# Performance work log

Hardware: AMD Instinct MI355X
Metric: run time of the kernel (lower is better)

The kernel has to match this reference:

```python
import jax, jax.numpy as jnp
import numpy as np

B, L, D, N = 2, 2048, 1024, 16
H = D // N  # head dim 64
MASK_FILL = -100000000.0  # torch code uses -1e8 for non-fp16


def sinusoidal_pos(seq_len, dim):
    # interleaved (sin, cos) table, shape (seq_len, dim); identical per head
    inv_freq = 1.0 / (10000.0 ** (jnp.arange(0, dim, 2, dtype=jnp.float32) / dim))
    ang = jnp.arange(seq_len, dtype=jnp.float32)[:, None] * inv_freq[None, :]
    return jnp.stack([jnp.sin(ang), jnp.cos(ang)], axis=-1).reshape(seq_len, dim)


def apply_rope(x, pos_emb):
    # x: (b, n, l, h); pos_emb: (l, h) interleaved sin/cos
    cos = jnp.repeat(pos_emb[..., 1::2], 2, axis=-1)  # (l, h)
    sin = jnp.repeat(pos_emb[..., ::2], 2, axis=-1)
    x2 = jnp.stack([-x[..., 1::2], x[..., ::2]], axis=-1).reshape(x.shape)
    return x * cos + x2 * sin


def setup_inputs() -> dict:
    key = jax.random.key(0)
    ks = jax.random.split(key, 12)
    inp = {
        "q": jax.random.normal(ks[0], (B, L, D), dtype=jnp.float32),
        "k": jax.random.normal(ks[1], (B, L, D), dtype=jnp.float32),
        "v": jax.random.normal(ks[2], (B, L, D), dtype=jnp.float32),
        "mask": jax.random.bernoulli(ks[3], 0.3, (B, L)),  # True = masked
    }
    s = 0.02
    for i, name in enumerate(["q", "k", "v", "o"]):
        inp[f"W{name}"] = jax.random.normal(ks[4 + i], (D, D), dtype=jnp.float32) * s
        inp[f"b{name}"] = jax.random.normal(ks[8 + i], (D,), dtype=jnp.float32) * s
    return inp


def reference(q, k, v, mask, Wq, bq, Wk, bk, Wv, bv, Wo, bo):
    # projections (torch Linear: x @ W^T + b) and head split -> (b, n, l, h)
    def split_heads(x):
        return x.reshape(B, L, N, H).transpose(0, 2, 1, 3)

    qw = split_heads(q @ Wq.T + bq)
    kw = split_heads(k @ Wk.T + bk)
    vw = split_heads(v @ Wv.T + bv)

    pos = sinusoidal_pos(L, H)
    qw = apply_rope(qw, pos)
    kw = apply_rope(kw, pos)

    # NOTE: original scales by sqrt(hidden_dim), not sqrt(head_dim)
    scores = jnp.einsum("bnlh,bnph->bnlp", qw, kw) / np.sqrt(D).astype(np.float32)
    scores = jnp.where(mask[:, None, None, :], MASK_FILL, scores)
    attn = jax.nn.softmax(scores, axis=-1)  # dropout is identity in eval

    out = jnp.einsum("bnlp,bnph->bnlh", attn, vw)  # (b, n, l, h)
    out = out.transpose(0, 2, 1, 3).reshape(B, L, D)
    return out @ Wo.T + bo
```

## Files before the change

kernel.cpp:

```cpp
#include <hip/hip_runtime.h>
#include <stdint.h>

#define L_SEQ 2048
#define DMODEL 1024
#define NHEAD 16
#define HDIM 64
#define BATCH 2

typedef __attribute__((ext_vector_type(8))) short bf16x8;
typedef __attribute__((ext_vector_type(4))) float f32x4;

#define MFMA(a, b, c) __builtin_amdgcn_mfma_f32_16x16x32_bf16((a), (b), (c), 0, 0, 0)

#if __has_builtin(__builtin_amdgcn_exp2f)
#define EXP2(x) __builtin_amdgcn_exp2f(x)
#else
#define EXP2(x) exp2f(x)
#endif

#if __has_builtin(__builtin_amdgcn_wave_barrier)
#define WAVE_FENCE() __builtin_amdgcn_wave_barrier()
#else
#define WAVE_FENCE() __syncthreads()
#endif

#define QSCALE 0.04508422f
#define MASKBIAS -100.0f

__device__ __forceinline__ unsigned short f2bf(float f) {
    return (unsigned short)((__float_as_uint(f) + 0x8000u) >> 16);
}
__device__ __forceinline__ float bf2f(unsigned short h) {
    return __uint_as_float(((unsigned int)h) << 16);
}
__device__ __forceinline__ unsigned int pkbf(float a, float b) {
    return __builtin_amdgcn_perm(__float_as_uint(b) + 0x8000u,
                                 __float_as_uint(a) + 0x8000u, 0x07060302u);
}
__device__ __forceinline__ void gl2lds16(const unsigned short* g, unsigned short* l) {
    __builtin_amdgcn_global_load_lds(
        (const __attribute__((address_space(1))) void*)g,
        (__attribute__((address_space(3))) void*)l, 16, 0, 0);
}

__global__ void prep_kernel(
    const float* __restrict__ q, const float* __restrict__ k, const float* __restrict__ v,
    const float* __restrict__ wq, const float* __restrict__ wk, const float* __restrict__ wv,
    const float* __restrict__ Wo, const int* __restrict__ mask,
    unsigned short* __restrict__ xb, unsigned short* __restrict__ wb,
    unsigned short* __restrict__ whi, unsigned short* __restrict__ wlo,
    float2* __restrict__ ropetab, float* __restrict__ fbias)
{
    const int y = blockIdx.y, x = blockIdx.x, tid = threadIdx.x;
    if (y < 6) {
        const float* src = (y == 0) ? q : (y == 1) ? k : (y == 2) ? v
                         : (y == 3) ? wq : (y == 4) ? wk : wv;
        unsigned short* dst = (y < 3) ? xb + (size_t)y * 4194304
                                      : wb + (size_t)(y - 3) * 1048576;
        const int n = (y < 3) ? 4194304 : 1048576;
        const int i = (x * 256 + tid) * 8;
        if (i >= n) return;
        const float4 a = *(const float4*)(src + i);
        const float4 b = *(const float4*)(src + i + 4);
        uint4 u;
        u.x = pkbf(a.x, a.y); u.y = pkbf(a.z, a.w);
        u.z = pkbf(b.x, b.y); u.w = pkbf(b.z, b.w);
        *(uint4*)(dst + i) = u;
    } else if (y == 6) {
        const int i = (x * 256 + tid) * 4;
        if (i >= DMODEL * DMODEL) return;
        const float4 vv = *(const float4*)(Wo + i);
        const float f[4] = {vv.x, vv.y, vv.z, vv.w};
        union { unsigned short s[4]; uint2 u; } h, l;
#pragma unroll
        for (int r = 0; r < 4; ++r) {
            h.s[r] = f2bf(f[r]);
            l.s[r] = f2bf(f[r] - bf2f(h.s[r]));
        }
        *(uint2*)&whi[i] = h.u;
        *(uint2*)&wlo[i] = l.u;
    } else {
        if (x < 512) {
            const int idx = x * 256 + tid;
            const int l = idx >> 6, h = idx & 63;
            const float invf = powf(10000.0f, -(float)(h & 62) * (1.0f / 64.0f));
            float sn, cs;
            sincosf((float)l * invf, &sn, &cs);
            ropetab[idx] = make_float2(cs, sn);
        } else if (x < 528) {
            const int idx = (x - 512) * 256 + tid;
            fbias[idx] = (mask[idx] != 0) ? MASKBIAS : 0.0f;
        }
    }
}

__global__ __launch_bounds__(256) void qkv_kernel(
    const unsigned short* __restrict__ Xb, const unsigned short* __restrict__ Wb,
    const float* __restrict__ bq, const float* __restrict__ bk, const float* __restrict__ bv,
    const float2* __restrict__ ropetab,
    unsigned short* __restrict__ Qd, unsigned short* __restrict__ Kd,
    unsigned short* __restrict__ Vd)
{
    const int id = blockIdx.x;
    const int bx = id / 96, rem = id % 96;
    const int z = rem >> 5, by = rem & 31;

    const unsigned short* X = Xb + (size_t)z * (BATCH * L_SEQ * DMODEL);
    const unsigned short* W = Wb + (size_t)z * (DMODEL * DMODEL);
    const float* bias = (z == 0) ? bq : (z == 1) ? bk : bv;

    __shared__ __align__(16) unsigned short As[128 * 64];
    __shared__ __align__(16) unsigned short Bs[128 * 64];

    const int tid  = threadIdx.x;
    const int wave = tid >> 6, lane = tid & 63;
    const int ml = lane & 15, kq = lane >> 4;
    const int m0 = by * 128, n0 = bx * 128;
    const int wm = (wave & 1) * 64, wn = (wave >> 1) * 64;

    f32x4 acc[4][4];
#pragma unroll
    for (int i = 0; i < 4; ++i)
#pragma unroll
        for (int j = 0; j < 4; ++j) acc[i][j] = (f32x4){0.f, 0.f, 0.f, 0.f};

    const int prow = wave * 32 + (lane >> 3);
    const int pch  = (lane & 7) ^ ((lane >> 3) & 7);
    const unsigned short* gA = X + (size_t)(m0 + prow) * DMODEL + pch * 8;
    const unsigned short* gB = W + (size_t)(n0 + prow) * DMODEL + pch * 8;
    unsigned short* lA = As + wave * 2048;
    unsigned short* lB = Bs + wave * 2048;

    for (int kc = 0; kc < DMODEL; kc += 64) {
#pragma unroll
        for (int qq = 0; qq < 4; ++qq) {
            gl2lds16(gA + kc + (size_t)qq * 8 * DMODEL, lA + qq * 512);
            gl2lds16(gB + kc + (size_t)qq * 8 * DMODEL, lB + qq * 512);
        }
        __syncthreads();

        bf16x8 af[2][4], bfv[2][4];
#pragma unroll
        for (int ks = 0; ks < 2; ++ks)
#pragma unroll
            for (int i = 0; i < 4; ++i) {
                const int Ra = wm + i * 16 + ml;
                af[ks][i] = *(const bf16x8*)&As[Ra * 64 + (((ks * 4 + kq) ^ (Ra & 7)) << 3)];
                const int Rb = wn + i * 16 + ml;
                bfv[ks][i] = *(const bf16x8*)&Bs[Rb * 64 + (((ks * 4 + kq) ^ (Rb & 7)) << 3)];
            }
#pragma unroll
        for (int ks = 0; ks < 2; ++ks)
#pragma unroll
            for (int i = 0; i < 4; ++i)
#pragma unroll
                for (int j = 0; j < 4; ++j)
                    acc[i][j] = MFMA(af[ks][i], bfv[ks][j], acc[i][j]);
        __syncthreads();
    }

    if (z < 2) {
        unsigned short* dst = (z == 0) ? Qd : Kd;
        const float osc = (z == 0) ? QSCALE : 1.0f;
#pragma unroll
        for (int jt = 0; jt < 4; ++jt) {
            const int col = n0 + wn + jt * 16 + ml;
            const float bv = bias[col];
            const int nh = col >> 6, hh = col & 63;
            const int odd = hh & 1;
#pragma unroll
            for (int it = 0; it < 4; ++it) {
#pragma unroll
                for (int r = 0; r < 4; ++r) {
                    const int row = m0 + wm + it * 16 + kq * 4 + r;
                    const int bb = row >> 11, ll = row & 2047;
                    const float v = acc[it][jt][r] + bv;
                    const float partner = __shfl_xor(v, 1);
                    const float2 cs = ropetab[ll * 64 + hh];
                    const float res = odd ? fmaf(v, cs.x, partner * cs.y)
                                          : fmaf(v, cs.x, -partner * cs.y);
                    dst[(((size_t)(bb * NHEAD + nh) * L_SEQ + ll) << 6) + hh] = f2bf(res * osc);
                }
            }
        }
    } else {
#pragma unroll
        for (int jt = 0; jt < 4; ++jt) {
            const int col = n0 + wn + jt * 16 + ml;
            const float bv = bias[col];
            const int nh = col >> 6, hh = col & 63;
#pragma unroll
            for (int it = 0; it < 4; ++it) {
                const int rb = m0 + wm + it * 16 + kq * 4;
                const int bb = rb >> 11, ll = rb & 2047;
                uint2 pk;
                pk.x = pkbf(acc[it][jt][0] + bv, acc[it][jt][1] + bv);
                pk.y = pkbf(acc[it][jt][2] + bv, acc[it][jt][3] + bv);
                *(uint2*)&Vd[(((size_t)bb * NHEAD + nh) * HDIM + hh) * L_SEQ + ll] = pk;
            }
        }
    }
}

__global__ __launch_bounds__(256) void attn_kernel(
    const unsigned short* __restrict__ Qr, const unsigned short* __restrict__ Kr,
    const unsigned short* __restrict__ Vt, const float* __restrict__ fbias,
    unsigned short* __restrict__ AOhi, unsigned short* __restrict__ AOlo)
{
    __shared__ __align__(16) unsigned short Ks[2][64 * 64];
    __shared__ __align__(16) unsigned short Vs[2][64 * 64];
    __shared__ __align__(16) unsigned short Ps[4][32 * 64];

    const int tid  = threadIdx.x;
    const int wave = tid >> 6, lane = tid & 63;
    const int ml = lane & 15, kq = lane >> 4;

    const int id = blockIdx.x;
    const int xcd = id & 7, slot = id >> 3;
    const int bh = xcd * 4 + (slot & 3);
    const int qb = slot >> 2;
    const int b = bh >> 4, nh = bh & 15;
    const int q0 = qb * 128;
    const int wq = wave * 32;

    const unsigned short* Qp = Qr + (size_t)bh * L_SEQ * HDIM;
    const unsigned short* Kp = Kr + (size_t)bh * L_SEQ * HDIM;
    const unsigned short* Vp = Vt + (size_t)bh * HDIM * L_SEQ;

    bf16x8 qf[2][2];
#pragma unroll
    for (int qt = 0; qt < 2; ++qt)
#pragma unroll
        for (int c = 0; c < 2; ++c)
            qf[qt][c] = *(const bf16x8*)(Qp + (size_t)(q0 + wq + qt * 16 + ml) * HDIM + c * 32 + kq * 8);

    float li[2] = {0.f, 0.f};
    f32x4 o[2][4];
#pragma unroll
    for (int qt = 0; qt < 2; ++qt)
#pragma unroll
        for (int ht = 0; ht < 4; ++ht) o[qt][ht] = (f32x4){0.f, 0.f, 0.f, 0.f};

    unsigned short* Pw = Ps[wave];

    const int srow8 = lane >> 3;
    const int sch   = (lane & 7) ^ srow8;
    const unsigned short* gK = Kp + (size_t)(wave * 16 + srow8) * HDIM + sch * 8;
    const unsigned short* gV = Vp + (size_t)(wave * 16 + srow8) * L_SEQ + sch * 8;

#define STAGE(kt, bf)                                                          \
    do {                                                                       \
        gl2lds16(gK + (size_t)((kt) * 64) * HDIM, &Ks[bf][(wave * 16) * 64]);  \
        gl2lds16(gK + (size_t)((kt) * 64 + 8) * HDIM,                          \
                 &Ks[bf][(wave * 16 + 8) * 64]);                               \
        gl2lds16(gV + (kt) * 64, &Vs[bf][(wave * 16) * 64]);                   \
        gl2lds16(gV + (size_t)8 * L_SEQ + (kt) * 64,                           \
                 &Vs[bf][(wave * 16 + 8) * 64]);                               \
    } while (0)

    const float* fbp = fbias + (size_t)b * L_SEQ + kq * 4;
    f32x4 bcur[4], bnext[4];
#pragma unroll
    for (int nt = 0; nt < 4; ++nt) bcur[nt] = *(const f32x4*)(fbp + nt * 16);

    STAGE(0, 0);

    for (int kt = 0; kt < L_SEQ / 64; ++kt) {
        const int buf = kt & 1;
        __syncthreads();
        if (kt + 1 < L_SEQ / 64) {
            STAGE(kt + 1, buf ^ 1);
#pragma unroll
            for (int nt = 0; nt < 4; ++nt)
                bnext[nt] = *(const f32x4*)(fbp + (kt + 1) * 64 + nt * 16);
        }

        const unsigned short* Kb = Ks[buf];
        const unsigned short* Vb = Vs[buf];

        f32x4 st[2][4];
#pragma unroll
        for (int nt = 0; nt < 4; ++nt) {
            const int R = nt * 16 + ml;
            const bf16x8 kf0 = *(const bf16x8*)&Kb[R * 64 + ((kq ^ (R & 7)) << 3)];
            const bf16x8 kf1 = *(const bf16x8*)&Kb[R * 64 + (((4 + kq) ^ (R & 7)) << 3)];
#pragma unroll
            for (int qt = 0; qt < 2; ++qt) {
                f32x4 c = MFMA(kf0, qf[qt][0], bcur[nt]);
                c = MFMA(kf1, qf[qt][1], c);
                st[qt][nt] = c;
            }
        }

#pragma unroll
        for (int qt = 0; qt < 2; ++qt) {
#pragma unroll
            for (int nt = 0; nt < 4; ++nt) {
                float p[4];
#pragma unroll
                for (int r = 0; r < 4; ++r) {
                    p[r] = EXP2(st[qt][nt][r]);
                    li[qt] += p[r];
                }
                uint2 pk;
                pk.x = pkbf(p[0], p[1]);
                pk.y = pkbf(p[2], p[3]);
                const int row = qt * 16 + ml;
                const int ck = nt * 2 + (kq >> 1);
                *(uint2*)&Pw[row * 64 + ((ck ^ (ml & 7)) << 3) + (kq & 1) * 4] = pk;
            }
        }
        WAVE_FENCE();

        bf16x8 pf[2][2];
#pragma unroll
        for (int qt = 0; qt < 2; ++qt) {
            const int row = qt * 16 + ml;
            pf[qt][0] = *(const bf16x8*)&Pw[row * 64 + ((kq ^ (ml & 7)) << 3)];
            pf[qt][1] = *(const bf16x8*)&Pw[row * 64 + (((4 + kq) ^ (ml & 7)) << 3)];
        }
#pragma unroll
        for (int ht = 0; ht < 4; ++ht) {
            const int R = ht * 16 + ml;
            const bf16x8 vf0 = *(const bf16x8*)&Vb[R * 64 + ((kq ^ (R & 7)) << 3)];
            const bf16x8 vf1 = *(const bf16x8*)&Vb[R * 64 + (((4 + kq) ^ (R & 7)) << 3)];
#pragma unroll
            for (int qt = 0; qt < 2; ++qt) {
                o[qt][ht] = MFMA(vf0, pf[qt][0], o[qt][ht]);
                o[qt][ht] = MFMA(vf1, pf[qt][1], o[qt][ht]);
            }
        }
        WAVE_FENCE();

#pragma unroll
        for (int nt = 0; nt < 4; ++nt) bcur[nt] = bnext[nt];
    }
#undef STAGE

#pragma unroll
    for (int qt = 0; qt < 2; ++qt) {
        li[qt] += __shfl_xor(li[qt], 16);
        li[qt] += __shfl_xor(li[qt], 32);
    }
    const float inv[2] = {1.f / li[0], 1.f / li[1]};

    const int qr = lane >> 2, quarter = lane & 3;
    const int rc0 = (quarter * 2) ^ (qr & 7), rc1 = (quarter * 2 + 1) ^ (qr & 7);

#pragma unroll
    for (int qt = 0; qt < 2; ++qt)
#pragma unroll
        for (int ht = 0; ht < 4; ++ht) {
            uint2 pk;
            pk.x = pkbf(o[qt][ht][0] * inv[qt], o[qt][ht][1] * inv[qt]);
            pk.y = pkbf(o[qt][ht][2] * inv[qt], o[qt][ht][3] * inv[qt]);
            const int row = qt * 16 + ml;
            const int ck = ht * 2 + (kq >> 1);
            *(uint2*)&Pw[row * 64 + ((ck ^ (ml & 7)) << 3) + (kq & 1) * 4] = pk;
        }
    WAVE_FENCE();
#pragma unroll
    for (int qt = 0; qt < 2; ++qt) {
        const size_t gbase = ((size_t)b * L_SEQ + q0 + wq + qt * 16 + qr) * DMODEL
                             + nh * 64 + quarter * 16;
        const uint4 d0 = *(const uint4*)&Pw[(qt * 16 + qr) * 64 + (rc0 << 3)];
        const uint4 d1 = *(const uint4*)&Pw[(qt * 16 + qr) * 64 + (rc1 << 3)];
        *(uint4*)&AOhi[gbase]     = d0;
        *(uint4*)&AOhi[gbase + 8] = d1;
    }
    WAVE_FENCE();
#pragma unroll
    for (int qt = 0; qt < 2; ++qt)
#pragma unroll
        for (int ht = 0; ht < 4; ++ht) {
            float lo[4];
#pragma unroll
            for (int r = 0; r < 4; ++r) {
                const float v = o[qt][ht][r] * inv[qt];
                const float hf = __uint_as_float((__float_as_uint(v) + 0x8000u) & 0xffff0000u);
                lo[r] = v - hf;
            }
            uint2 pk;
            pk.x = pkbf(lo[0], lo[1]);
            pk.y = pkbf(lo[2], lo[3]);
            const int row = qt * 16 + ml;
            const int ck = ht * 2 + (kq >> 1);
            *(uint2*)&Pw[row * 64 + ((ck ^ (ml & 7)) << 3) + (kq & 1) * 4] = pk;
        }
    WAVE_FENCE();
#pragma unroll
    for (int qt = 0; qt < 2; ++qt) {
        const size_t gbase = ((size_t)b * L_SEQ + q0 + wq + qt * 16 + qr) * DMODEL
                             + nh * 64 + quarter * 16;
        const uint4 d0 = *(const uint4*)&Pw[(qt * 16 + qr) * 64 + (rc0 << 3)];
        const uint4 d1 = *(const uint4*)&Pw[(qt * 16 + qr) * 64 + (rc1 << 3)];
        *(uint4*)&AOlo[gbase]     = d0;
        *(uint4*)&AOlo[gbase + 8] = d1;
    }
}

__global__ __launch_bounds__(256) void oproj_kernel(
    const unsigned short* __restrict__ Ahi_g, const unsigned short* __restrict__ Alo_g,
    const unsigned short* __restrict__ Whi_g, const unsigned short* __restrict__ Wlo_g,
    const float* __restrict__ bias, float* __restrict__ out)
{
    const int id = blockIdx.x;
    const int bxn = id >> 5, by = id & 31;

    __shared__ __align__(16) unsigned short Ah[128 * 32], Al[128 * 32];
    __shared__ __align__(16) unsigned short Bh[64 * 32],  Bl[64 * 32];

    const int tid  = threadIdx.x;
    const int wave = tid >> 6, lane = tid & 63;
    const int ml = lane & 15, kq = lane >> 4;
    const int m0 = by * 128, n0 = bxn * 64;
    const int wm = (wave & 1) * 64, wn = (wave >> 1) * 32;

    f32x4 acc[4][2];
#pragma unroll
    for (int i = 0; i < 4; ++i)
#pragma unroll
        for (int j = 0; j < 2; ++j) acc[i][j] = (f32x4){0.f, 0.f, 0.f, 0.f};

    const int rl  = lane >> 2;
    const int pch = (lane & 3) ^ ((lane >> 3) & 3);
    const int prowA = wave * 32 + rl;
    const int prowB = wave * 16 + rl;
    const unsigned short* gAh = Ahi_g + (size_t)(m0 + prowA) * DMODEL + pch * 8;
    const unsigned short* gAl = Alo_g + (size_t)(m0 + prowA) * DMODEL + pch * 8;
    const unsigned short* gBh = Whi_g + (size_t)(n0 + prowB) * DMODEL + pch * 8;
    const unsigned short* gBl = Wlo_g + (size_t)(n0 + prowB) * DMODEL + pch * 8;
    unsigned short* lAh = Ah + wave * 1024;
    unsigned short* lAl = Al + wave * 1024;
    unsigned short* lBh = Bh + wave * 512;
    unsigned short* lBl = Bl + wave * 512;

    for (int kc = 0; kc < DMODEL; kc += 32) {
#pragma unroll
        for (int qq = 0; qq < 2; ++qq) {
            const size_t go = kc + (size_t)qq * 16 * DMODEL;
            gl2lds16(gAh + go, lAh + qq * 512);
            gl2lds16(gAl + go, lAl + qq * 512);
        }
        gl2lds16(gBh + kc, lBh);
        gl2lds16(gBl + kc, lBl);
        __syncthreads();

        bf16x8 ah[4], al[4], bh_[2], bl_[2];
#pragma unroll
        for (int i = 0; i < 4; ++i) {
            const int Ra = wm + i * 16 + ml;
            const int sa = Ra * 32 + ((kq ^ ((Ra >> 1) & 3)) << 3);
            ah[i] = *(const bf16x8*)&Ah[sa];
            al[i] = *(const bf16x8*)&Al[sa];
        }
#pragma unroll
        for (int j = 0; j < 2; ++j) {
            const int Rb = wn + j * 16 + ml;
            const int sb = Rb * 32 + ((kq ^ ((Rb >> 1) & 3)) << 3);
            bh_[j] = *(const bf16x8*)&Bh[sb];
            bl_[j] = *(const bf16x8*)&Bl[sb];
        }
#pragma unroll
        for (int i = 0; i < 4; ++i)
#pragma unroll
            for (int j = 0; j < 2; ++j) {
                acc[i][j] = MFMA(ah[i], bh_[j], acc[i][j]);
                acc[i][j] = MFMA(al[i], bh_[j], acc[i][j]);
                acc[i][j] = MFMA(ah[i], bl_[j], acc[i][j]);
            }
        __syncthreads();
    }

#pragma unroll
    for (int jt = 0; jt < 2; ++jt) {
        const int col = n0 + wn + jt * 16 + ml;
        const float bv = bias[col];
#pragma unroll
        for (int it = 0; it < 4; ++it)
#pragma unroll
            for (int r = 0; r < 4; ++r) {
                const int row = m0 + wm + it * 16 + kq * 4 + r;
                out[(size_t)row * DMODEL + col] = acc[it][jt][r] + bv;
            }
    }
}

extern "C" void kernel_launch(void* const* d_in, const int* in_sizes, int n_in,
                              void* d_out, int out_size, void* d_ws, size_t ws_size,
                              hipStream_t stream)
{
    (void)in_sizes; (void)n_in; (void)out_size; (void)ws_size;
    const float* q    = (const float*)d_in[0];
    const float* k    = (const float*)d_in[1];
    const float* v    = (const float*)d_in[2];
    const int*   mask = (const int*)d_in[3];
    const float* Wq   = (const float*)d_in[4];
    const float* bq   = (const float*)d_in[5];
    const float* Wk   = (const float*)d_in[6];
    const float* bk   = (const float*)d_in[7];
    const float* Wv   = (const float*)d_in[8];
    const float* bv   = (const float*)d_in[9];
    const float* Wo   = (const float*)d_in[10];
    const float* bo   = (const float*)d_in[11];
    float* out = (float*)d_out;

    const size_t HE = (size_t)BATCH * NHEAD * L_SEQ * HDIM;
    const size_t DD = (size_t)DMODEL * DMODEL;
    unsigned short* Xb   = (unsigned short*)d_ws;
    unsigned short* Wb   = Xb + 3 * HE;
    unsigned short* Qr   = Wb + 3 * DD;
    unsigned short* Kr   = Qr + HE;
    unsigned short* Vt   = Kr + HE;
    unsigned short* Whi  = Vt + HE;
    unsigned short* Wlo  = Whi + DD;
    float* fbias = (float*)(Wlo + DD);
    float2* ropetab = (float2*)(fbias + (size_t)BATCH * L_SEQ);
    unsigned short* AOhi = Xb;
    unsigned short* AOlo = Xb + HE;

    prep_kernel<<<dim3(2048, 8), dim3(256), 0, stream>>>(
        q, k, v, Wq, Wk, Wv, Wo, mask, Xb, Wb, Whi, Wlo, ropetab, fbias);

    qkv_kernel<<<dim3(768), dim3(256), 0, stream>>>(Xb, Wb, bq, bk, bv, ropetab, Qr, Kr, Vt);

    attn_kernel<<<dim3(512), dim3(256), 0, stream>>>(Qr, Kr, Vt, fbias, AOhi, AOlo);

    oproj_kernel<<<dim3(512), dim3(256), 0, stream>>>(AOhi, AOlo, Whi, Wlo, bo, out);
}
```

Before: 248.9 us.

## Split attention over key dimension with atomic accumulation and separate normalize kernel

Result: slower. 351.0 us (+41.1%).

```diff
diff --git a/kernel.cpp b/kernel.cpp
--- a/kernel.cpp
+++ b/kernel.cpp
@@ -6,6 +6,8 @@
 #define NHEAD 16
 #define HDIM 64
 #define BATCH 2
+#define KSPLIT 2
+#define NKT (L_SEQ / 64 / KSPLIT)
 
 typedef __attribute__((ext_vector_type(8))) short bf16x8;
 typedef __attribute__((ext_vector_type(4))) float f32x4;
@@ -94,6 +96,20 @@
     }
 }
 
+__global__ __launch_bounds__(256) void zero_kernel(
+    float* __restrict__ accum, float* __restrict__ liacc)
+{
+    const size_t NA = (size_t)BATCH * NHEAD * L_SEQ * HDIM;
+    const size_t NL = (size_t)BATCH * NHEAD * L_SEQ;
+    const size_t i = ((size_t)blockIdx.x * 256 + threadIdx.x) * 4;
+    if (i < NA) {
+        *(float4*)(accum + i) = make_float4(0.f, 0.f, 0.f, 0.f);
+    } else {
+        const size_t j = i - NA;
+        if (j < NL) *(float4*)(liacc + j) = make_float4(0.f, 0.f, 0.f, 0.f);
+    }
+}
+
 __global__ __launch_bounds__(256) void qkv_kernel(
     const unsigned short* __restrict__ Xb, const unsigned short* __restrict__ Wb,
     const float* __restrict__ bq, const float* __restrict__ bk, const float* __restrict__ bv,
@@ -205,7 +221,7 @@
 __global__ __launch_bounds__(256) void attn_kernel(
     const unsigned short* __restrict__ Qr, const unsigned short* __restrict__ Kr,
     const unsigned short* __restrict__ Vt, const float* __restrict__ fbias,
-    unsigned short* __restrict__ AOhi, unsigned short* __restrict__ AOlo)
+    float* __restrict__ accum, float* __restrict__ liacc)
 {
     __shared__ __align__(16) unsigned short Ks[2][64 * 64];
     __shared__ __align__(16) unsigned short Vs[2][64 * 64];
@@ -216,12 +232,15 @@
     const int ml = lane & 15, kq = lane >> 4;
 
     const int id = blockIdx.x;
-    const int xcd = id & 7, slot = id >> 3;
+    const int sp  = id >> 9;
+    const int rid = id & 511;
+    const int xcd = rid & 7, slot = rid >> 3;
     const int bh = xcd * 4 + (slot & 3);
     const int qb = slot >> 2;
-    const int b = bh >> 4, nh = bh & 15;
+    const int b = bh >> 4;
     const int q0 = qb * 128;
     const int wq = wave * 32;
+    const int koff = sp * (L_SEQ / KSPLIT);
 
     const unsigned short* Qp = Qr + (size_t)bh * L_SEQ * HDIM;
     const unsigned short* Kp = Kr + (size_t)bh * L_SEQ * HDIM;
@@ -245,8 +264,8 @@
 
     const int srow8 = lane >> 3;
     const int sch   = (lane & 7) ^ srow8;
-    const unsigned short* gK = Kp + (size_t)(wave * 16 + srow8) * HDIM + sch * 8;
-    const unsigned short* gV = Vp + (size_t)(wave * 16 + srow8) * L_SEQ + sch * 8;
+    const unsigned short* gK = Kp + (size_t)(koff + wave * 16 + srow8) * HDIM + sch * 8;
+    const unsigned short* gV = Vp + (size_t)(wave * 16 + srow8) * L_SEQ + koff + sch * 8;
 
 #define STAGE(kt, bf)                                                          \
     do {                                                                       \
@@ -258,17 +277,17 @@
                  &Vs[bf][(wave * 16 + 8) * 64]);                               \
     } while (0)
 
-    const float* fbp = fbias + (size_t)b * L_SEQ + kq * 4;
+    const float* fbp = fbias + (size_t)b * L_SEQ + koff + kq * 4;
     f32x4 bcur[4], bnext[4];
 #pragma unroll
     for (int nt = 0; nt < 4; ++nt) bcur[nt] = *(const f32x4*)(fbp + nt * 16);
 
     STAGE(0, 0);
 
-    for (int kt = 0; kt < L_SEQ / 64; ++kt) {
+    for (int kt = 0; kt < NKT; ++kt) {
         const int buf = kt & 1;
         __syncthreads();
-        if (kt + 1 < L_SEQ / 64) {
+        if (kt + 1 < NKT) {
             STAGE(kt + 1, buf ^ 1);
 #pragma unroll
             for (int nt = 0; nt < 4; ++nt)
@@ -342,60 +361,46 @@
         li[qt] += __shfl_xor(li[qt], 16);
         li[qt] += __shfl_xor(li[qt], 32);
     }
-    const float inv[2] = {1.f / li[0], 1.f / li[1]};
-
-    const int qr = lane >> 2, quarter = lane & 3;
-    const int rc0 = (quarter * 2) ^ (qr & 7), rc1 = (quarter * 2 + 1) ^ (qr & 7);
-
-#pragma unroll
-    for (int qt = 0; qt < 2; ++qt)
+
+    float* accb = accum + ((size_t)bh * L_SEQ + q0 + wq) * HDIM;
+#pragma unroll
+    for (int qt = 0; qt < 2; ++qt) {
 #pragma unroll
         for (int ht = 0; ht < 4; ++ht) {
-            uint2 pk;
-            pk.x = pkbf(o[qt][ht][0] * inv[qt], o[qt][ht][1] * inv[qt]);
-            pk.y = pkbf(o[qt][ht][2] * inv[qt], o[qt][ht][3] * inv[qt]);
-            const int row = qt * 16 + ml;
-            const int ck = ht * 2 + (kq >> 1);
-            *(uint2*)&Pw[row * 64 + ((ck ^ (ml & 7)) << 3) + (kq & 1) * 4] = pk;
-        }
-    WAVE_FENCE();
-#pragma unroll
-    for (int qt = 0; qt < 2; ++qt) {
-        const size_t gbase = ((size_t)b * L_SEQ + q0 + wq + qt * 16 + qr) * DMODEL
-                             + nh * 64 + quarter * 16;
-        const uint4 d0 = *(const uint4*)&Pw[(qt * 16 + qr) * 64 + (rc0 << 3)];
-        const uint4 d1 = *(const uint4*)&Pw[(qt * 16 + qr) * 64 + (rc1 << 3)];
-        *(uint4*)&AOhi[gbase]     = d0;
-        *(uint4*)&AOhi[gbase + 8] = d1;
-    }
-    WAVE_FENCE();
-#pragma unroll
-    for (int qt = 0; qt < 2; ++qt)
-#pragma unroll
-        for (int ht = 0; ht < 4; ++ht) {
-            float lo[4];
-#pragma unroll
-            for (int r = 0; r < 4; ++r) {
-                const float v = o[qt][ht][r] * inv[qt];
-                const float hf = __uint_as_float((__float_as_uint(v) + 0x8000u) & 0xffff0000u);
-                lo[r] = v - hf;
-            }
-            uint2 pk;
-            pk.x = pkbf(lo[0], lo[1]);
-            pk.y = pkbf(lo[2], lo[3]);
-            const int row = qt * 16 + ml;
-            const int ck = ht * 2 + (kq >> 1);
-            *(uint2*)&Pw[row * 64 + ((ck ^ (ml & 7)) << 3) + (kq & 1) * 4] = pk;
-        }
-    WAVE_FENCE();
-#pragma unroll
-    for (int qt = 0; qt < 2; ++qt) {
-        const size_t gbase = ((size_t)b * L_SEQ + q0 + wq + qt * 16 + qr) * DMODEL
-                             + nh * 64 + quarter * 16;
-        const uint4 d0 = *(const uint4*)&Pw[(qt * 16 + qr) * 64 + (rc0 << 3)];
-        const uint4 d1 = *(const uint4*)&Pw[(qt * 16 + qr) * 64 + (rc1 << 3)];
-        *(uint4*)&AOlo[gbase]     = d0;
-        *(uint4*)&AOlo[gbase + 8] = d1;
+            const int base = (qt * 16 + ml) * HDIM + ht * 16 + kq * 4;
+#pragma unroll
+            for (int r = 0; r < 4; ++r)
+                atomicAdd(accb + base + r, o[qt][ht][r]);
+        }
+    }
+    if (kq == 0) {
+#pragma unroll
+        for (int qt = 0; qt < 2; ++qt)
+            atomicAdd(liacc + (size_t)bh * L_SEQ + q0 + wq + qt * 16 + ml, li[qt]);
+    }
+}
+
+__global__ __launch_bounds__(256) void norm_kernel(
+    const float* __restrict__ accum, const float* __restrict__ liacc,
+    unsigned short* __restrict__ AOhi, unsigned short* __restrict__ AOlo)
+{
+    const int id = blockIdx.x;
+    const int bh = id >> 4, qb = id & 15;
+    const int b = bh >> 4, nh = bh & 15;
+    const int t = threadIdx.x;
+    const int h = t & 63, qq = t >> 6;
+    const float* ap = accum + ((size_t)bh * L_SEQ + qb * 128) * HDIM;
+    const float* lp = liacc + (size_t)bh * L_SEQ + qb * 128;
+#pragma unroll 4
+    for (int p = 0; p < 32; ++p) {
+        const int ql = p * 4 + qq;
+        const float inv = 1.0f / lp[ql];
+        const float v = ap[ql * 64 + h] * inv;
+        const unsigned short hi = f2bf(v);
+        const unsigned short lo = f2bf(v - bf2f(hi));
+        const size_t g = ((size_t)b * L_SEQ + qb * 128 + ql) * DMODEL + nh * 64 + h;
+        AOhi[g] = hi;
+        AOlo[g] = lo;
     }
 }
 
@@ -516,15 +521,22 @@
     unsigned short* Wlo  = Whi + DD;
     float* fbias = (float*)(Wlo + DD);
     float2* ropetab = (float2*)(fbias + (size_t)BATCH * L_SEQ);
-    unsigned short* AOhi = Xb;
-    unsigned short* AOlo = Xb + HE;
+    float* liacc = (float*)(ropetab + (size_t)L_SEQ * 64);
+
+    float* accum = (float*)Xb;
+    unsigned short* AOhi = Xb + 2 * HE;
+    unsigned short* AOlo = Qr;
 
     prep_kernel<<<dim3(2048, 8), dim3(256), 0, stream>>>(
         q, k, v, Wq, Wk, Wv, Wo, mask, Xb, Wb, Whi, Wlo, ropetab, fbias);
 
     qkv_kernel<<<dim3(768), dim3(256), 0, stream>>>(Xb, Wb, bq, bk, bv, ropetab, Qr, Kr, Vt);
 
-    attn_kernel<<<dim3(512), dim3(256), 0, stream>>>(Qr, Kr, Vt, fbias, AOhi, AOlo);
+    zero_kernel<<<dim3(4160), dim3(256), 0, stream>>>(accum, liacc);
+
+    attn_kernel<<<dim3(1024), dim3(256), 0, stream>>>(Qr, Kr, Vt, fbias, accum, liacc);
+
+    norm_kernel<<<dim3(512), dim3(256), 0, stream>>>(accum, liacc, AOhi, AOlo);
 
     oproj_kernel<<<dim3(512), dim3(256), 0, stream>>>(AOhi, AOlo, Whi, Wlo, bo, out);
 }
```

## Split attention KV range across two wave groups and merge partials in LDS

Applied to the files above, without the earlier changes.

Measured after the change: 246.5 us. No clear change (-0.9%).

```diff
diff --git a/kernel.cpp b/kernel.cpp
--- a/kernel.cpp
+++ b/kernel.cpp
@@ -6,6 +6,9 @@
 #define NHEAD 16
 #define HDIM 64
 #define BATCH 2
+#define KVBLK 32
+#define KHALF (L_SEQ / 2)
+#define NKT (KHALF / KVBLK)
 
 typedef __attribute__((ext_vector_type(8))) short bf16x8;
 typedef __attribute__((ext_vector_type(4))) float f32x4;
@@ -202,17 +205,16 @@
     }
 }
 
-__global__ __launch_bounds__(256) void attn_kernel(
+__global__ __launch_bounds__(512, 4) void attn_kernel(
     const unsigned short* __restrict__ Qr, const unsigned short* __restrict__ Kr,
     const unsigned short* __restrict__ Vt, const float* __restrict__ fbias,
     unsigned short* __restrict__ AOhi, unsigned short* __restrict__ AOlo)
 {
-    __shared__ __align__(16) unsigned short Ks[2][64 * 64];
-    __shared__ __align__(16) unsigned short Vs[2][64 * 64];
-    __shared__ __align__(16) unsigned short Ps[4][32 * 64];
+    __shared__ __align__(16) unsigned short lds[24832];
 
     const int tid  = threadIdx.x;
-    const int wave = tid >> 6, lane = tid & 63;
+    const int w    = tid >> 6, lane = tid & 63;
+    const int kh   = w >> 2, qg = w & 3;
     const int ml = lane & 15, kq = lane >> 4;
 
     const int id = blockIdx.x;
@@ -221,7 +223,8 @@
     const int qb = slot >> 2;
     const int b = bh >> 4, nh = bh & 15;
     const int q0 = qb * 128;
-    const int wq = wave * 32;
+    const int wq = qg * 32;
+    const int koff = kh * KHALF;
 
     const unsigned short* Qp = Qr + (size_t)bh * L_SEQ * HDIM;
     const unsigned short* Kp = Kr + (size_t)bh * L_SEQ * HDIM;
@@ -241,46 +244,46 @@
 #pragma unroll
         for (int ht = 0; ht < 4; ++ht) o[qt][ht] = (f32x4){0.f, 0.f, 0.f, 0.f};
 
-    unsigned short* Pw = Ps[wave];
+    unsigned short* Pw = lds + 16384 + w * 1024;
 
     const int srow8 = lane >> 3;
     const int sch   = (lane & 7) ^ srow8;
-    const unsigned short* gK = Kp + (size_t)(wave * 16 + srow8) * HDIM + sch * 8;
-    const unsigned short* gV = Vp + (size_t)(wave * 16 + srow8) * L_SEQ + sch * 8;
-
-#define STAGE(kt, bf)                                                          \
-    do {                                                                       \
-        gl2lds16(gK + (size_t)((kt) * 64) * HDIM, &Ks[bf][(wave * 16) * 64]);  \
-        gl2lds16(gK + (size_t)((kt) * 64 + 8) * HDIM,                          \
-                 &Ks[bf][(wave * 16 + 8) * 64]);                               \
-        gl2lds16(gV + (kt) * 64, &Vs[bf][(wave * 16) * 64]);                   \
-        gl2lds16(gV + (size_t)8 * L_SEQ + (kt) * 64,                           \
-                 &Vs[bf][(wave * 16 + 8) * 64]);                               \
+    const unsigned short* gK = Kp + (size_t)(koff + qg * 8 + srow8) * HDIM + sch * 8;
+    const int vrow = lane >> 2;
+    const int vch  = (lane & 3) ^ (vrow & 3);
+    const unsigned short* gV = Vp + (size_t)(qg * 16 + vrow) * L_SEQ + koff + vch * 8;
+
+#define STAGE(kt, bf)                                                           \
+    do {                                                                        \
+        gl2lds16(gK + (size_t)(kt) * KVBLK * HDIM,                              \
+                 lds + ((bf) * 2 + kh) * 2048 + qg * 512);                      \
+        gl2lds16(gV + (kt) * KVBLK,                                             \
+                 lds + 8192 + ((bf) * 2 + kh) * 2048 + qg * 512);               \
     } while (0)
 
-    const float* fbp = fbias + (size_t)b * L_SEQ + kq * 4;
-    f32x4 bcur[4], bnext[4];
-#pragma unroll
-    for (int nt = 0; nt < 4; ++nt) bcur[nt] = *(const f32x4*)(fbp + nt * 16);
+    const float* fbp = fbias + (size_t)b * L_SEQ + koff + kq * 4;
+    f32x4 bcur[2], bnext[2];
+#pragma unroll
+    for (int nt = 0; nt < 2; ++nt) bcur[nt] = *(const f32x4*)(fbp + nt * 16);
 
     STAGE(0, 0);
 
-    for (int kt = 0; kt < L_SEQ / 64; ++kt) {
+    for (int kt = 0; kt < NKT; ++kt) {
         const int buf = kt & 1;
         __syncthreads();
-        if (kt + 1 < L_SEQ / 64) {
+        if (kt + 1 < NKT) {
             STAGE(kt + 1, buf ^ 1);
 #pragma unroll
-            for (int nt = 0; nt < 4; ++nt)
-                bnext[nt] = *(const f32x4*)(fbp + (kt + 1) * 64 + nt * 16);
-        }
-
-        const unsigned short* Kb = Ks[buf];
-        const unsigned short* Vb = Vs[buf];
-
-        f32x4 st[2][4];
-#pragma unroll
-        for (int nt = 0; nt < 4; ++nt) {
+            for (int nt = 0; nt < 2; ++nt)
+                bnext[nt] = *(const f32x4*)(fbp + (kt + 1) * KVBLK + nt * 16);
+        }
+
+        const unsigned short* Kb = lds + (buf * 2 + kh) * 2048;
+        const unsigned short* Vb = lds + 8192 + (buf * 2 + kh) * 2048;
+
+        f32x4 st[2][2];
+#pragma unroll
+        for (int nt = 0; nt < 2; ++nt) {
             const int R = nt * 16 + ml;
             const bf16x8 kf0 = *(const bf16x8*)&Kb[R * 64 + ((kq ^ (R & 7)) << 3)];
             const bf16x8 kf1 = *(const bf16x8*)&Kb[R * 64 + (((4 + kq) ^ (R & 7)) << 3)];
@@ -295,7 +298,7 @@
 #pragma unroll
         for (int qt = 0; qt < 2; ++qt) {
 #pragma unroll
-            for (int nt = 0; nt < 4; ++nt) {
+            for (int nt = 0; nt < 2; ++nt) {
                 float p[4];
 #pragma unroll
                 for (int r = 0; r < 4; ++r) {
@@ -306,34 +309,30 @@
                 pk.x = pkbf(p[0], p[1]);
                 pk.y = pkbf(p[2], p[3]);
                 const int row = qt * 16 + ml;
-                const int ck = nt * 2 + (kq >> 1);
-                *(uint2*)&Pw[row * 64 + ((ck ^ (ml & 7)) << 3) + (kq & 1) * 4] = pk;
+                const int cg = (nt * 2 + (kq >> 1)) ^ (row & 3);
+                *(uint2*)&Pw[row * 32 + (cg << 3) + (kq & 1) * 4] = pk;
             }
         }
         WAVE_FENCE();
 
-        bf16x8 pf[2][2];
+        bf16x8 pf[2];
 #pragma unroll
         for (int qt = 0; qt < 2; ++qt) {
             const int row = qt * 16 + ml;
-            pf[qt][0] = *(const bf16x8*)&Pw[row * 64 + ((kq ^ (ml & 7)) << 3)];
-            pf[qt][1] = *(const bf16x8*)&Pw[row * 64 + (((4 + kq) ^ (ml & 7)) << 3)];
+            pf[qt] = *(const bf16x8*)&Pw[row * 32 + ((kq ^ (row & 3)) << 3)];
         }
 #pragma unroll
         for (int ht = 0; ht < 4; ++ht) {
             const int R = ht * 16 + ml;
-            const bf16x8 vf0 = *(const bf16x8*)&Vb[R * 64 + ((kq ^ (R & 7)) << 3)];
-            const bf16x8 vf1 = *(const bf16x8*)&Vb[R * 64 + (((4 + kq) ^ (R & 7)) << 3)];
-#pragma unroll
-            for (int qt = 0; qt < 2; ++qt) {
-                o[qt][ht] = MFMA(vf0, pf[qt][0], o[qt][ht]);
-                o[qt][ht] = MFMA(vf1, pf[qt][1], o[qt][ht]);
-            }
+            const bf16x8 vf = *(const bf16x8*)&Vb[R * 32 + ((kq ^ (R & 3)) << 3)];
+#pragma unroll
+            for (int qt = 0; qt < 2; ++qt)
+                o[qt][ht] = MFMA(vf, pf[qt], o[qt][ht]);
         }
         WAVE_FENCE();
 
 #pragma unroll
-        for (int nt = 0; nt < 4; ++nt) bcur[nt] = bnext[nt];
+        for (int nt = 0; nt < 2; ++nt) bcur[nt] = bnext[nt];
     }
 #undef STAGE
 
@@ -342,8 +341,34 @@
         li[qt] += __shfl_xor(li[qt], 16);
         li[qt] += __shfl_xor(li[qt], 32);
     }
+
+    float* osc = (float*)lds;
+    float* lis = (float*)(lds + 24576);
+    __syncthreads();
+    if (kh == 1) {
+#pragma unroll
+        for (int qt = 0; qt < 2; ++qt)
+#pragma unroll
+            for (int ht = 0; ht < 4; ++ht)
+                *(f32x4*)(osc + qg * 2048 + (qt * 4 + ht) * 256 + lane * 4) = o[qt][ht];
+        if (kq == 0) {
+            lis[qg * 32 + ml]      = li[0];
+            lis[qg * 32 + 16 + ml] = li[1];
+        }
+    }
+    __syncthreads();
+    if (kh == 1) return;
+
+#pragma unroll
+    for (int qt = 0; qt < 2; ++qt) {
+#pragma unroll
+        for (int ht = 0; ht < 4; ++ht)
+            o[qt][ht] += *(const f32x4*)(osc + qg * 2048 + (qt * 4 + ht) * 256 + lane * 4);
+        li[qt] += lis[qg * 32 + qt * 16 + ml];
+    }
     const float inv[2] = {1.f / li[0], 1.f / li[1]};
 
+    unsigned short* Pe = lds + 16384 + qg * 2048;
     const int qr = lane >> 2, quarter = lane & 3;
     const int rc0 = (quarter * 2) ^ (qr & 7), rc1 = (quarter * 2 + 1) ^ (qr & 7);
 
@@ -356,15 +381,15 @@
             pk.y = pkbf(o[qt][ht][2] * inv[qt], o[qt][ht][3] * inv[qt]);
             const int row = qt * 16 + ml;
             const int ck = ht * 2 + (kq >> 1);
-            *(uint2*)&Pw[row * 64 + ((ck ^ (ml & 7)) << 3) + (kq & 1) * 4] = pk;
+            *(uint2*)&Pe[row * 64 + ((ck ^ (ml & 7)) << 3) + (kq & 1) * 4] = pk;
         }
     WAVE_FENCE();
 #pragma unroll
     for (int qt = 0; qt < 2; ++qt) {
         const size_t gbase = ((size_t)b * L_SEQ + q0 + wq + qt * 16 + qr) * DMODEL
                              + nh * 64 + quarter * 16;
-        const uint4 d0 = *(const uint4*)&Pw[(qt * 16 + qr) * 64 + (rc0 << 3)];
-        const uint4 d1 = *(const uint4*)&Pw[(qt * 16 + qr) * 64 + (rc1 << 3)];
+        const uint4 d0 = *(const uint4*)&Pe[(qt * 16 + qr) * 64 + (rc0 << 3)];
+        const uint4 d1 = *(const uint4*)&Pe[(qt * 16 + qr) * 64 + (rc1 << 3)];
         *(uint4*)&AOhi[gbase]     = d0;
         *(uint4*)&AOhi[gbase + 8] = d1;
     }
@@ -385,15 +410,15 @@
             pk.y = pkbf(lo[2], lo[3]);
             const int row = qt * 16 + ml;
             const int ck = ht * 2 + (kq >> 1);
-            *(uint2*)&Pw[row * 64 + ((ck ^ (ml & 7)) << 3) + (kq & 1) * 4] = pk;
+            *(uint2*)&Pe[row * 64 + ((ck ^ (ml & 7)) << 3) + (kq & 1) * 4] = pk;
         }
     WAVE_FENCE();
 #pragma unroll
     for (int qt = 0; qt < 2; ++qt) {
         const size_t gbase = ((size_t)b * L_SEQ + q0 + wq + qt * 16 + qr) * DMODEL
                              + nh * 64 + quarter * 16;
-        const uint4 d0 = *(const uint4*)&Pw[(qt * 16 + qr) * 64 + (rc0 << 3)];
-        const uint4 d1 = *(const uint4*)&Pw[(qt * 16 + qr) * 64 + (rc1 << 3)];
+        const uint4 d0 = *(const uint4*)&Pe[(qt * 16 + qr) * 64 + (rc0 << 3)];
+        const uint4 d1 = *(const uint4*)&Pe[(qt * 16 + qr) * 64 + (rc1 << 3)];
         *(uint4*)&AOlo[gbase]     = d0;
         *(uint4*)&AOlo[gbase + 8] = d1;
     }
@@ -524,7 +549,7 @@
 
     qkv_kernel<<<dim3(768), dim3(256), 0, stream>>>(Xb, Wb, bq, bk, bv, ropetab, Qr, Kr, Vt);
 
-    attn_kernel<<<dim3(512), dim3(256), 0, stream>>>(Qr, Kr, Vt, fbias, AOhi, AOlo);
+    attn_kernel<<<dim3(512), dim3(512), 0, stream>>>(Qr, Kr, Vt, fbias, AOhi, AOlo);
 
     oproj_kernel<<<dim3(512), dim3(256), 0, stream>>>(AOhi, AOlo, Whi, Wlo, bo, out);
 }
```
